# Kernel tuning notes

Hardware: AMD Instinct MI355X
Metric: run time of the kernel (lower is better)

## Reference

```python
import jax, jax.numpy as jnp
import numpy as np

# Standard 24-joint SMPL kinematic tree (parent indices), root has parent -1.
PARENTS = [-1, 0, 0, 0, 1, 2, 3, 4, 5, 6, 7, 8, 9, 9, 9, 12, 13, 14, 16, 17, 18, 19, 20, 21]
NUM_JOINTS = len(PARENTS)
BATCH = 524288


def setup_inputs() -> dict:
    key = jax.random.key(0)
    k1, k2 = jax.random.split(key)
    orientations = jax.random.normal(k1, (BATCH, NUM_JOINTS, 3, 3), dtype=jnp.float32)
    offsets = jax.random.normal(k2, (NUM_JOINTS, 3), dtype=jnp.float32) * 0.1
    return {"orientations": orientations, "offsets": offsets}


def reference(orientations, offsets):
    # to_mvnx frame change: R' = G^T @ R @ G with fixed axis-permutation G
    G = jnp.array([[0.0, 1.0, 0.0], [0.0, 0.0, 1.0], [1.0, 0.0, 0.0]], dtype=jnp.float32)
    ori = jnp.einsum('ji,bnjk,kl->bnil', G, orientations, G)  # [B, J, 3, 3]
    B = orientations.shape[0]
    # Sequential tree FK: pos[i] = pos[parent] + R_parent @ offset_i
    # (structural loop over the fixed 24-joint topology; vectorized over batch)
    positions = [None] * NUM_JOINTS
    positions[0] = jnp.zeros((B, 3), dtype=jnp.float32)  # root stays at origin
    for i, p in enumerate(PARENTS):
        if p == -1:
            continue
        positions[i] = positions[p] + jnp.einsum('bij,j->bi', ori[:, p], offsets[i])
    pos = jnp.stack(positions, axis=1)  # [B, J, 3]
    # to_smpl frame change: rotate every position vector by R (same matrix as G)
    return jnp.einsum('ij,bnj->bni', G, pos)  # [B, J, 3]
```

## Files before the change

### kernel.cpp

```cpp
#include <hip/hip_runtime.h>


#define NJ 24

typedef const __attribute__((address_space(1))) void* gptr_t;
typedef __attribute__((address_space(3))) void* lptr_t;

__global__ __launch_bounds__(64, 2) void fk_kernel(
    const float* __restrict__ ori,
    const float* __restrict__ off,
    float* __restrict__ out,
    int B)
{
    const int l = threadIdx.x;
    const long long tile = blockIdx.x;
    const float* __restrict__ gbase = ori + tile * (64LL * 216);

    __shared__ alignas(16) float4 s4[64 * 45];

#pragma unroll
    for (int i = 0; i < 45; ++i) {
        const unsigned idx = (unsigned)(i * 64 + l);
        const unsigned row = idx / 45u;
        const unsigned w   = idx - row * 45u;
        const unsigned g   = (w < 23u) ? w
                           : (w < 30u) ? (w + 4u)
                           : (w < 44u) ? (w + 6u)
                           : 0u;
        const float* src = gbase + ((size_t)row * 54u + g) * 4u;
        __builtin_amdgcn_global_load_lds((gptr_t)src, (lptr_t)(&s4[i * 64]),
                                         16, 0, 0);
    }
    __syncthreads();

    const float4* __restrict__ rbase = &s4[l * 45];

    float qx[NJ], qy[NJ], qz[NJ];
    qx[0] = 0.0f; qy[0] = 0.0f; qz[0] = 0.0f;

    float r[9];

#define LOADM(o) { \
    const float4 w0 = rbase[(o)/4 + 0]; \
    const float4 w1 = rbase[(o)/4 + 1]; \
    const float4 w2 = rbase[(o)/4 + 2]; \
    const float tt[12] = {w0.x,w0.y,w0.z,w0.w, w1.x,w1.y,w1.z,w1.w, \
                          w2.x,w2.y,w2.z,w2.w}; \
    r[0]=tt[(o)%4+0]; r[1]=tt[(o)%4+1]; r[2]=tt[(o)%4+2]; \
    r[3]=tt[(o)%4+3]; r[4]=tt[(o)%4+4]; r[5]=tt[(o)%4+5]; \
    r[6]=tt[(o)%4+6]; r[7]=tt[(o)%4+7]; r[8]=tt[(o)%4+8]; }

#define CHILD(p, c) { \
    const float vx = off[3*(c)+1]; \
    const float vy = off[3*(c)+2]; \
    const float vz = off[3*(c)+0]; \
    qx[c] = fmaf(r[0], vx, fmaf(r[1], vy, fmaf(r[2], vz, qx[p]))); \
    qy[c] = fmaf(r[3], vx, fmaf(r[4], vy, fmaf(r[5], vz, qy[p]))); \
    qz[c] = fmaf(r[6], vx, fmaf(r[7], vy, fmaf(r[8], vz, qz[p]))); }

    LOADM(0);   CHILD(0, 1);  CHILD(0, 2);  CHILD(0, 3);
    LOADM(9);   CHILD(1, 4);
    LOADM(18);  CHILD(2, 5);
    LOADM(27);  CHILD(3, 6);
    LOADM(36);  CHILD(4, 7);
    LOADM(45);  CHILD(5, 8);
    LOADM(54);  CHILD(6, 9);
    LOADM(63);  CHILD(7, 10);
    LOADM(72);  CHILD(8, 11);
    LOADM(81);  CHILD(9, 12); CHILD(9, 13); CHILD(9, 14);
    LOADM(92);  CHILD(12, 15);
    LOADM(101); CHILD(13, 16);
    LOADM(110); CHILD(14, 17);
    LOADM(120); CHILD(16, 18);
    LOADM(129); CHILD(17, 19);
    LOADM(138); CHILD(18, 20);
    LOADM(147); CHILD(19, 21);
    LOADM(156); CHILD(20, 22);
    LOADM(165); CHILD(21, 23);
#undef LOADM
#undef CHILD

    float fv[72];
#pragma unroll
    for (int i = 0; i < NJ; ++i) {
        fv[3*i+0] = qx[i];
        fv[3*i+1] = qy[i];
        fv[3*i+2] = qz[i];
    }

    __syncthreads();

    float4* __restrict__ so4 = (float4*)s4;
#pragma unroll
    for (int j = 0; j < 18; ++j)
        so4[l * 19 + j] = make_float4(fv[4*j+0], fv[4*j+1], fv[4*j+2], fv[4*j+3]);

    __syncthreads();

    float4* __restrict__ o4 = (float4*)(out + tile * (64LL * 72));
#pragma unroll
    for (int j = 0; j < 18; ++j) {
        const unsigned g2   = (unsigned)(j * 64 + l);
        const unsigned row2 = g2 / 18u;
        const unsigned w2   = g2 - row2 * 18u;
        o4[g2] = so4[row2 * 19u + w2];
    }
}

extern "C" void kernel_launch(void* const* d_in, const int* in_sizes, int n_in,
                              void* d_out, int out_size, void* d_ws, size_t ws_size,
                              hipStream_t stream) {
    const float* ori = (const float*)d_in[0];
    const float* off = (const float*)d_in[1];
    float* out = (float*)d_out;

    int B = in_sizes[0] / 216;
    dim3 block(64);
    dim3 grid(B / 64);
    hipLaunchKernelGGL(fk_kernel, grid, block, 0, stream, ori, off, out, B);
}
```

Measured before the change: 122.1 us.

## Split matrix staging into two phases to halve LDS footprint

Row data is now staged through LDS in two passes of 23 and 21 float4 per row, each followed by the part of the FK chain it feeds. The old single pass staged 45 float4 per row. This cuts the shared buffer from 45 to 23 float4 per thread, and the launch-bounds minimum-blocks hint is dropped. The aim is more resident workgroups per CU to hide memory latency, at the cost of extra barriers and less load overlap inside each block.

```diff
diff --git a/kernel.cpp b/kernel.cpp
--- a/kernel.cpp
+++ b/kernel.cpp
@@ -6,7 +6,7 @@
 typedef const __attribute__((address_space(1))) void* gptr_t;
 typedef __attribute__((address_space(3))) void* lptr_t;
 
-__global__ __launch_bounds__(64, 2) void fk_kernel(
+__global__ __launch_bounds__(64) void fk_kernel(
     const float* __restrict__ ori,
     const float* __restrict__ off,
     float* __restrict__ out,
@@ -16,34 +16,15 @@
     const long long tile = blockIdx.x;
     const float* __restrict__ gbase = ori + tile * (64LL * 216);
 
-    __shared__ alignas(16) float4 s4[64 * 45];
-
-#pragma unroll
-    for (int i = 0; i < 45; ++i) {
-        const unsigned idx = (unsigned)(i * 64 + l);
-        const unsigned row = idx / 45u;
-        const unsigned w   = idx - row * 45u;
-        const unsigned g   = (w < 23u) ? w
-                           : (w < 30u) ? (w + 4u)
-                           : (w < 44u) ? (w + 6u)
-                           : 0u;
-        const float* src = gbase + ((size_t)row * 54u + g) * 4u;
-        __builtin_amdgcn_global_load_lds((gptr_t)src, (lptr_t)(&s4[i * 64]),
-                                         16, 0, 0);
-    }
-    __syncthreads();
-
-    const float4* __restrict__ rbase = &s4[l * 45];
+    __shared__ alignas(16) float4 s4[64 * 23];
 
     float qx[NJ], qy[NJ], qz[NJ];
     qx[0] = 0.0f; qy[0] = 0.0f; qz[0] = 0.0f;
 
-    float r[9];
-
-#define LOADM(o) { \
-    const float4 w0 = rbase[(o)/4 + 0]; \
-    const float4 w1 = rbase[(o)/4 + 1]; \
-    const float4 w2 = rbase[(o)/4 + 2]; \
+#define LOADM(RB, o) { \
+    const float4 w0 = (RB)[(o)/4 + 0]; \
+    const float4 w1 = (RB)[(o)/4 + 1]; \
+    const float4 w2 = (RB)[(o)/4 + 2]; \
     const float tt[12] = {w0.x,w0.y,w0.z,w0.w, w1.x,w1.y,w1.z,w1.w, \
                           w2.x,w2.y,w2.z,w2.w}; \
     r[0]=tt[(o)%4+0]; r[1]=tt[(o)%4+1]; r[2]=tt[(o)%4+2]; \
@@ -58,25 +39,58 @@
     qy[c] = fmaf(r[3], vx, fmaf(r[4], vy, fmaf(r[5], vz, qy[p]))); \
     qz[c] = fmaf(r[6], vx, fmaf(r[7], vy, fmaf(r[8], vz, qz[p]))); }
 
-    LOADM(0);   CHILD(0, 1);  CHILD(0, 2);  CHILD(0, 3);
-    LOADM(9);   CHILD(1, 4);
-    LOADM(18);  CHILD(2, 5);
-    LOADM(27);  CHILD(3, 6);
-    LOADM(36);  CHILD(4, 7);
-    LOADM(45);  CHILD(5, 8);
-    LOADM(54);  CHILD(6, 9);
-    LOADM(63);  CHILD(7, 10);
-    LOADM(72);  CHILD(8, 11);
-    LOADM(81);  CHILD(9, 12); CHILD(9, 13); CHILD(9, 14);
-    LOADM(92);  CHILD(12, 15);
-    LOADM(101); CHILD(13, 16);
-    LOADM(110); CHILD(14, 17);
-    LOADM(120); CHILD(16, 18);
-    LOADM(129); CHILD(17, 19);
-    LOADM(138); CHILD(18, 20);
-    LOADM(147); CHILD(19, 21);
-    LOADM(156); CHILD(20, 22);
-    LOADM(165); CHILD(21, 23);
+#pragma unroll
+    for (int i = 0; i < 23; ++i) {
+        const unsigned idx = (unsigned)(i * 64 + l);
+        const unsigned row = idx / 23u;
+        const unsigned w   = idx - row * 23u;
+        const float* src = gbase + (size_t)row * 216u + (size_t)w * 4u;
+        __builtin_amdgcn_global_load_lds((gptr_t)src, (lptr_t)(&s4[i * 64]),
+                                         16, 0, 0);
+    }
+    __syncthreads();
+
+    {
+        const float4* __restrict__ rb = &s4[l * 23];
+        float r[9];
+        LOADM(rb, 0);   CHILD(0, 1);  CHILD(0, 2);  CHILD(0, 3);
+        LOADM(rb, 9);   CHILD(1, 4);
+        LOADM(rb, 18);  CHILD(2, 5);
+        LOADM(rb, 27);  CHILD(3, 6);
+        LOADM(rb, 36);  CHILD(4, 7);
+        LOADM(rb, 45);  CHILD(5, 8);
+        LOADM(rb, 54);  CHILD(6, 9);
+        LOADM(rb, 63);  CHILD(7, 10);
+        LOADM(rb, 72);  CHILD(8, 11);
+        LOADM(rb, 81);  CHILD(9, 12); CHILD(9, 13); CHILD(9, 14);
+    }
+    __syncthreads();
+
+#pragma unroll
+    for (int i = 0; i < 21; ++i) {
+        const unsigned idx = (unsigned)(i * 64 + l);
+        const unsigned row = idx / 21u;
+        const unsigned w   = idx - row * 21u;
+        const unsigned g   = (w < 7u) ? (w + 27u) : (w + 29u);
+        const float* src = gbase + (size_t)row * 216u + (size_t)g * 4u;
+        __builtin_amdgcn_global_load_lds((gptr_t)src, (lptr_t)(&s4[i * 64]),
+                                         16, 0, 0);
+    }
+    __syncthreads();
+
+    {
+        const float4* __restrict__ rb = &s4[l * 21];
+        float r[9];
+        LOADM(rb, 0);   CHILD(12, 15);
+        LOADM(rb, 9);   CHILD(13, 16);
+        LOADM(rb, 18);  CHILD(14, 17);
+        LOADM(rb, 28);  CHILD(16, 18);
+        LOADM(rb, 37);  CHILD(17, 19);
+        LOADM(rb, 46);  CHILD(18, 20);
+        LOADM(rb, 55);  CHILD(19, 21);
+        LOADM(rb, 64);  CHILD(20, 22);
+        LOADM(rb, 73);  CHILD(21, 23);
+    }
 #undef LOADM
 #undef CHILD
 
```

Result: faster. 119.7 us (-2.0%).
